# Performance work log

Measured on AMD Instinct MI355X. Metric: run time of the kernel, lower is better.

Reference implementation:

```python
import jax, jax.numpy as jnp
import numpy as np

INPUT_DIM = 512
HIDDEN_DIM = 512

def setup_inputs() -> dict:
    key = jax.random.key(0)
    ks = jax.random.split(key, 7)
    B, S = 4, 4096
    s = 1.0 / np.sqrt(INPUT_DIM)
    return {
        "x": jax.random.normal(ks[0], (B, INPUT_DIM, S), dtype=jnp.float32),
        "Wq": jax.random.uniform(ks[1], (INPUT_DIM, HIDDEN_DIM), jnp.float32, -s, s),
        "bq": jax.random.uniform(ks[2], (HIDDEN_DIM,), jnp.float32, -s, s),
        "Wk": jax.random.uniform(ks[3], (INPUT_DIM, HIDDEN_DIM), jnp.float32, -s, s),
        "bk": jax.random.uniform(ks[4], (HIDDEN_DIM,), jnp.float32, -s, s),
        "Wv": jax.random.uniform(ks[5], (INPUT_DIM, HIDDEN_DIM), jnp.float32, -s, s),
        "bv": jax.random.uniform(ks[6], (HIDDEN_DIM,), jnp.float32, -s, s),
    }

def reference(x, Wq, bq, Wk, bk, Wv, bv):
    # x: [B, input_dim, S] -> [B, S, input_dim]
    xt = jnp.swapaxes(x, 1, 2)
    q = xt @ Wq + bq  # [B, S, H]
    k = xt @ Wk + bk
    v = xt @ Wv + bv
    scale = 1.0 / jnp.sqrt(jnp.float32(HIDDEN_DIM))
    scores = jnp.einsum('bsh,bth->bst', q, k) * scale  # [B, S, S]
    attn = jax.nn.softmax(scores, axis=-1)
    out = jnp.einsum('bst,bth->bsh', attn, v)  # [B, S, H]
    return jnp.swapaxes(out, 1, 2)  # [B, H, S]
```

## Files before the change

### kernel.cpp

```cpp
#include <hip/hip_runtime.h>
#include <stdint.h>
#include <stddef.h>

typedef __attribute__((ext_vector_type(8))) short bf16x8;
typedef __attribute__((ext_vector_type(4))) short bf16x4;
typedef __attribute__((ext_vector_type(4))) float f32x4;

#define MFMA16x16x32 __builtin_amdgcn_mfma_f32_16x16x32_bf16
#define L2E 1.4426950408889634f

#define GLD_LDS(gp, lp)                                                              \
  __builtin_amdgcn_global_load_lds((const __attribute__((address_space(1))) void*)(gp), \
                                   (__attribute__((address_space(3))) void*)(lp), 16, 0, 0)

__device__ __forceinline__ short f2bf(float f) {
  union { float f; uint32_t u; } c; c.f = f;
  uint32_t r = c.u + 0x7fffu + ((c.u >> 16) & 1u);
  return (short)(r >> 16);
}

__global__ __launch_bounds__(256) void k_transpose_x(const float* __restrict__ x,
                                                     short* __restrict__ xt) {
  __shared__ float tile[32][33];
  const int b = blockIdx.z;
  const int s0 = blockIdx.x * 32, k0 = blockIdx.y * 32;
  const int tx = threadIdx.x, ty = threadIdx.y;
  const float* xp = x + ((size_t)b * 512 + k0) * 4096 + s0;
#pragma unroll
  for (int i = 0; i < 32; i += 8) tile[ty + i][tx] = xp[(size_t)(ty + i) * 4096 + tx];
  __syncthreads();
  short* op = xt + ((size_t)b * 4096 + s0) * 512 + k0;
#pragma unroll
  for (int i = 0; i < 32; i += 8) op[(size_t)(ty + i) * 512 + tx] = f2bf(tile[tx][ty + i]);
}

__global__ __launch_bounds__(256) void k_transpose_w(const float* __restrict__ w,
                                                     short* __restrict__ wt, float scale) {
  __shared__ float tile[32][33];
  const int h0 = blockIdx.x * 32, k0 = blockIdx.y * 32;
  const int tx = threadIdx.x, ty = threadIdx.y;
#pragma unroll
  for (int i = 0; i < 32; i += 8) tile[ty + i][tx] = w[(size_t)(k0 + ty + i) * 512 + h0 + tx];
  __syncthreads();
#pragma unroll
  for (int i = 0; i < 32; i += 8)
    wt[(size_t)(h0 + ty + i) * 512 + k0 + tx] = f2bf(tile[tx][ty + i] * scale);
}

__global__ __launch_bounds__(256) void k_proj_gemm(const short* __restrict__ A,
                                                   const short* __restrict__ Bt,
                                                   const float* __restrict__ bias,
                                                   short* __restrict__ outp,
                                                   float bscale, int vmode) {
  __shared__ short As[128 * 64];
  __shared__ short Bs[128 * 64];
  const int tid = threadIdx.x, lane = tid & 63, wave = tid >> 6;
  const int m0 = blockIdx.x * 128, h0 = blockIdx.y * 128;
  const int wm = wave >> 1, wn = wave & 1;

  f32x4 acc[4][4];
#pragma unroll
  for (int fh = 0; fh < 4; ++fh) {
    float bv = bias[h0 + 64 * wn + 16 * fh + (lane & 15)] * bscale;
#pragma unroll
    for (int fm = 0; fm < 4; ++fm) acc[fm][fh] = (f32x4){bv, bv, bv, bv};
  }

  for (int k0 = 0; k0 < 512; k0 += 64) {
#pragma unroll
    for (int it = 0; it < 4; ++it) {
      int p = it * 256 + tid;
      int row = p >> 3;
      int c = p & 7;
      int pc = c ^ (row & 7);
      bf16x8 va = *(const bf16x8*)(A + (size_t)(m0 + row) * 512 + k0 + c * 8);
      bf16x8 vb = *(const bf16x8*)(Bt + (size_t)(h0 + row) * 512 + k0 + c * 8);
      *(bf16x8*)(As + row * 64 + pc * 8) = va;
      *(bf16x8*)(Bs + row * 64 + pc * 8) = vb;
    }
    __syncthreads();
#pragma unroll
    for (int kk = 0; kk < 2; ++kk) {
      bf16x8 af[4], bfr[4];
#pragma unroll
      for (int f = 0; f < 4; ++f) {
        int ra = 64 * wm + 16 * f + (lane & 15);
        int ca = (4 * kk + (lane >> 4)) ^ (ra & 7);
        af[f] = *(const bf16x8*)(As + ra * 64 + ca * 8);
        int rb = 64 * wn + 16 * f + (lane & 15);
        int cb = (4 * kk + (lane >> 4)) ^ (rb & 7);
        bfr[f] = *(const bf16x8*)(Bs + rb * 64 + cb * 8);
      }
#pragma unroll
      for (int fm = 0; fm < 4; ++fm)
#pragma unroll
        for (int fh = 0; fh < 4; ++fh)
          acc[fm][fh] = MFMA16x16x32(af[fm], bfr[fh], acc[fm][fh], 0, 0, 0);
    }
    __syncthreads();
  }

  if (vmode == 0) {
#pragma unroll
    for (int fm = 0; fm < 4; ++fm) {
      int rbase = m0 + 64 * wm + 16 * fm + (lane >> 4) * 4;
#pragma unroll
      for (int fh = 0; fh < 4; ++fh) {
        int h = h0 + 64 * wn + 16 * fh + (lane & 15);
#pragma unroll
        for (int j = 0; j < 4; ++j)
          outp[(size_t)(rbase + j) * 512 + h] = f2bf(acc[fm][fh][j]);
      }
    }
  } else {
#pragma unroll
    for (int fm = 0; fm < 4; ++fm) {
      int m = m0 + 64 * wm + 16 * fm + (lane >> 4) * 4;
      int b = m >> 12, s = m & 4095;
#pragma unroll
      for (int fh = 0; fh < 4; ++fh) {
        int h = h0 + 64 * wn + 16 * fh + (lane & 15);
        bf16x4 v;
#pragma unroll
        for (int j = 0; j < 4; ++j) v[j] = f2bf(acc[fm][fh][j]);
        *(bf16x4*)(outp + ((size_t)b * 512 + h) * 4096 + s) = v;
      }
    }
  }
}

__global__ __launch_bounds__(512) void k_attn(const short* __restrict__ Qg,
                                              const short* __restrict__ Kg,
                                              const short* __restrict__ VTg,
                                              float* __restrict__ out) {
  __shared__ short Ks[64 * 512];
  __shared__ short Vs[512 * 64];
  __shared__ short Pbuf[64 * 64];
  __shared__ float Lfin[64];

  const int tid = threadIdx.x, lane = tid & 63, wave = tid >> 6;
  const int hi = lane >> 4, lo = lane & 15;
  const int b = blockIdx.y, qb = blockIdx.x;
  const int s0 = qb * 64;
  const int wm = wave >> 2, st = wave & 3;

  const short* Qb = Qg + (size_t)b * 4096 * 512;
  const short* Kb = Kg + (size_t)b * 4096 * 512;
  const short* VTb = VTg + (size_t)b * 512 * 4096;

  const short* kSrc[8];
  const short* vSrc[8];
#pragma unroll
  for (int it = 0; it < 8; ++it) {
    int r = it * 8 + wave;
    kSrc[it] = Kb + (size_t)r * 512 + (lane ^ wave) * 8;
    int h = it * 64 + wave * 8 + (lane >> 3);
    int c = (lane & 7) ^ (lane >> 3);
    vSrc[it] = VTb + (size_t)h * 4096 + c * 8;
  }

  bf16x8 qreg[2][16];
#pragma unroll
  for (int fa = 0; fa < 2; ++fa) {
    const short* qp = Qb + (size_t)(s0 + 32 * wm + 16 * fa + lo) * 512 + 8 * hi;
#pragma unroll
    for (int c = 0; c < 16; ++c) qreg[fa][c] = *(const bf16x8*)(qp + 32 * c);
  }

  bf16x8 onesB;
#pragma unroll
  for (int j = 0; j < 8; ++j) onesB[j] = (short)0x3F80;

  f32x4 of[2][8];
#pragma unroll
  for (int i = 0; i < 2; ++i)
#pragma unroll
    for (int j = 0; j < 8; ++j) of[i][j] = (f32x4){0.f, 0.f, 0.f, 0.f};
  f32x4 ol[2];
  ol[0] = (f32x4){0.f, 0.f, 0.f, 0.f};
  ol[1] = (f32x4){0.f, 0.f, 0.f, 0.f};

#pragma unroll
  for (int it = 0; it < 8; ++it) GLD_LDS(kSrc[it], &Ks[(it * 8 + wave) * 512]);
#pragma unroll
  for (int it = 0; it < 8; ++it) GLD_LDS(vSrc[it], &Vs[it * 4096 + wave * 512]);
  asm volatile("s_waitcnt vmcnt(0)" ::: "memory");
  asm volatile("s_waitcnt lgkmcnt(0)" ::: "memory");
  __builtin_amdgcn_s_barrier();
  asm volatile("" ::: "memory");

  for (int t = 0; t < 64; ++t) {
    f32x4 sf[2];
    sf[0] = (f32x4){0.f, 0.f, 0.f, 0.f};
    sf[1] = (f32x4){0.f, 0.f, 0.f, 0.f};
    __builtin_amdgcn_s_setprio(1);
#pragma unroll
    for (int kk = 0; kk < 16; ++kk) {
      int r = 16 * st + lo;
      bf16x8 kb = *(const bf16x8*)(Ks + r * 512 + ((4 * kk + hi) ^ (r & 7)) * 8);
      sf[0] = MFMA16x16x32(qreg[0][kk], kb, sf[0], 0, 0, 0);
      sf[1] = MFMA16x16x32(qreg[1][kk], kb, sf[1], 0, 0, 0);
    }
    __builtin_amdgcn_s_setprio(0);

#pragma unroll
    for (int fa = 0; fa < 2; ++fa) {
      int chunk = 2 * st + (lo >> 3);
#pragma unroll
      for (int j = 0; j < 4; ++j) {
        int q = 32 * wm + 16 * fa + 4 * hi + j;
        float p = exp2f(sf[fa][j] * L2E);
        Pbuf[q * 64 + (chunk ^ (q & 7)) * 8 + (lo & 7)] = f2bf(p);
      }
    }
    asm volatile("s_waitcnt vmcnt(0)" ::: "memory");
    asm volatile("s_waitcnt lgkmcnt(0)" ::: "memory");
    __builtin_amdgcn_s_barrier();
    asm volatile("" ::: "memory");

    if (t < 63) {
#pragma unroll
      for (int it = 0; it < 8; ++it) {
        kSrc[it] += 64 * 512;
        GLD_LDS(kSrc[it], &Ks[(it * 8 + wave) * 512]);
      }
    }

    __builtin_amdgcn_s_setprio(1);
#pragma unroll
    for (int ks = 0; ks < 2; ++ks) {
      bf16x8 pa[2];
#pragma unroll
      for (int fm = 0; fm < 2; ++fm) {
        int r = 32 * wm + 16 * fm + lo;
        pa[fm] = *(const bf16x8*)(Pbuf + r * 64 + ((4 * ks + hi) ^ (r & 7)) * 8);
      }
#pragma unroll
      for (int fh = 0; fh < 8; ++fh) {
        int n = 128 * st + 16 * fh + lo;
        bf16x8 vb = *(const bf16x8*)(Vs + n * 64 + ((4 * ks + hi) ^ (n & 7)) * 8);
#pragma unroll
        for (int fm = 0; fm < 2; ++fm) of[fm][fh] = MFMA16x16x32(pa[fm], vb, of[fm][fh], 0, 0, 0);
      }
      if (st == 0) {
        ol[0] = MFMA16x16x32(pa[0], onesB, ol[0], 0, 0, 0);
        ol[1] = MFMA16x16x32(pa[1], onesB, ol[1], 0, 0, 0);
      }
    }
    __builtin_amdgcn_s_setprio(0);
    asm volatile("s_waitcnt vmcnt(0)" ::: "memory");
    asm volatile("s_waitcnt lgkmcnt(0)" ::: "memory");
    __builtin_amdgcn_s_barrier();
    asm volatile("" ::: "memory");

    if (t < 63) {
#pragma unroll
      for (int it = 0; it < 8; ++it) {
        vSrc[it] += 64;
        GLD_LDS(vSrc[it], &Vs[it * 4096 + wave * 512]);
      }
    }
  }

  if (st == 0 && lo == 0) {
#pragma unroll
    for (int fm = 0; fm < 2; ++fm)
#pragma unroll
      for (int j = 0; j < 4; ++j) Lfin[32 * wm + 16 * fm + 4 * hi + j] = ol[fm][j];
  }
  __syncthreads();

#pragma unroll
  for (int fm = 0; fm < 2; ++fm) {
    int rb2 = 32 * wm + 16 * fm + hi * 4;
    float inv[4];
#pragma unroll
    for (int j = 0; j < 4; ++j) inv[j] = 1.f / Lfin[rb2 + j];
#pragma unroll
    for (int fh = 0; fh < 8; ++fh) {
      int h = 128 * st + 16 * fh + lo;
      f32x4 v;
#pragma unroll
      for (int j = 0; j < 4; ++j) v[j] = of[fm][fh][j] * inv[j];
      *(f32x4*)(out + ((size_t)b * 512 + h) * 4096 + s0 + rb2) = v;
    }
  }
}

extern "C" void kernel_launch(void* const* d_in, const int* in_sizes, int n_in,
                              void* d_out, int out_size, void* d_ws, size_t ws_size,
                              hipStream_t stream) {
  (void)in_sizes; (void)n_in; (void)out_size; (void)ws_size;
  const float* x = (const float*)d_in[0];
  const float* Wq = (const float*)d_in[1];
  const float* bq = (const float*)d_in[2];
  const float* Wk = (const float*)d_in[3];
  const float* bk = (const float*)d_in[4];
  const float* Wv = (const float*)d_in[5];
  const float* bv = (const float*)d_in[6];
  float* out = (float*)d_out;
  char* ws = (char*)d_ws;

  short* xt  = (short*)(ws + 0);
  short* qg  = (short*)(ws + 16777216);
  short* kg  = (short*)(ws + 33554432);
  short* vtg = (short*)(ws + 50331648);
  short* wqt = (short*)(ws + 67108864);
  short* wkt = (short*)(ws + 67633152);
  short* wvt = (short*)(ws + 68157440);

  const float scale = 0.04419417382415922f;

  k_transpose_x<<<dim3(128, 16, 4), dim3(32, 8), 0, stream>>>(x, xt);
  k_transpose_w<<<dim3(16, 16), dim3(32, 8), 0, stream>>>(Wq, wqt, scale);
  k_transpose_w<<<dim3(16, 16), dim3(32, 8), 0, stream>>>(Wk, wkt, 1.0f);
  k_transpose_w<<<dim3(16, 16), dim3(32, 8), 0, stream>>>(Wv, wvt, 1.0f);

  k_proj_gemm<<<dim3(128, 4), 256, 0, stream>>>(xt, wqt, bq, qg, scale, 0);
  k_proj_gemm<<<dim3(128, 4), 256, 0, stream>>>(xt, wkt, bk, kg, 1.0f, 0);
  k_proj_gemm<<<dim3(128, 4), 256, 0, stream>>>(xt, wvt, bv, vtg, 1.0f, 1);

  k_attn<<<dim3(64, 4), 512, 0, stream>>>(qg, kg, vtg, out);
}
```

Before: 255.3 us.

## Load V fragments directly from global into registers instead of via LDS

Drops the shared-memory staging buffer for V. Each wave now reads its V^T fragments straight from global memory into registers inside the PV loop, and the per-iteration V prefetch into LDS is gone. K source pointers are recomputed from a single base instead of being kept in eight registers, and sched_barrier calls are added before the workgroup barriers. This halves LDS usage and removes LDS traffic for V, but global loads now sit on the critical path right before the MFMAs with no prefetch. It also relies on L2 to serve the four query-block reuses of V.

After: 452.6 us. 1.77x slower.

```diff
diff --git a/kernel.cpp b/kernel.cpp
--- a/kernel.cpp
+++ b/kernel.cpp
@@ -134,7 +134,6 @@
                                               const short* __restrict__ VTg,
                                               float* __restrict__ out) {
   __shared__ short Ks[64 * 512];
-  __shared__ short Vs[512 * 64];
   __shared__ short Pbuf[64 * 64];
   __shared__ float Lfin[64];
 
@@ -148,16 +147,8 @@
   const short* Kb = Kg + (size_t)b * 4096 * 512;
   const short* VTb = VTg + (size_t)b * 512 * 4096;
 
-  const short* kSrc[8];
-  const short* vSrc[8];
-#pragma unroll
-  for (int it = 0; it < 8; ++it) {
-    int r = it * 8 + wave;
-    kSrc[it] = Kb + (size_t)r * 512 + (lane ^ wave) * 8;
-    int h = it * 64 + wave * 8 + (lane >> 3);
-    int c = (lane & 7) ^ (lane >> 3);
-    vSrc[it] = VTb + (size_t)h * 4096 + c * 8;
-  }
+  const short* kSrcBase = Kb + (size_t)wave * 512 + (lane ^ wave) * 8;
+  const short* vBase = VTb + (size_t)(128 * st + lo) * 4096 + 8 * hi;
 
   bf16x8 qreg[2][16];
 #pragma unroll
@@ -181,11 +172,11 @@
   ol[1] = (f32x4){0.f, 0.f, 0.f, 0.f};
 
 #pragma unroll
-  for (int it = 0; it < 8; ++it) GLD_LDS(kSrc[it], &Ks[(it * 8 + wave) * 512]);
-#pragma unroll
-  for (int it = 0; it < 8; ++it) GLD_LDS(vSrc[it], &Vs[it * 4096 + wave * 512]);
+  for (int it = 0; it < 8; ++it)
+    GLD_LDS(kSrcBase + (size_t)it * 8 * 512, &Ks[(it * 8 + wave) * 512]);
   asm volatile("s_waitcnt vmcnt(0)" ::: "memory");
   asm volatile("s_waitcnt lgkmcnt(0)" ::: "memory");
+  __builtin_amdgcn_sched_barrier(0);
   __builtin_amdgcn_s_barrier();
   asm volatile("" ::: "memory");
 
@@ -215,20 +206,24 @@
     }
     asm volatile("s_waitcnt vmcnt(0)" ::: "memory");
     asm volatile("s_waitcnt lgkmcnt(0)" ::: "memory");
+    __builtin_amdgcn_sched_barrier(0);
     __builtin_amdgcn_s_barrier();
     asm volatile("" ::: "memory");
 
     if (t < 63) {
-#pragma unroll
-      for (int it = 0; it < 8; ++it) {
-        kSrc[it] += 64 * 512;
-        GLD_LDS(kSrc[it], &Ks[(it * 8 + wave) * 512]);
-      }
+      const short* kSrc = kSrcBase + (size_t)(t + 1) * 64 * 512;
+#pragma unroll
+      for (int it = 0; it < 8; ++it)
+        GLD_LDS(kSrc + (size_t)it * 8 * 512, &Ks[(it * 8 + wave) * 512]);
     }
 
     __builtin_amdgcn_s_setprio(1);
 #pragma unroll
     for (int ks = 0; ks < 2; ++ks) {
+      bf16x8 vb[8];
+#pragma unroll
+      for (int fh = 0; fh < 8; ++fh)
+        vb[fh] = *(const bf16x8*)(vBase + (size_t)fh * 16 * 4096 + 64 * t + 32 * ks);
       bf16x8 pa[2];
 #pragma unroll
       for (int fm = 0; fm < 2; ++fm) {
@@ -236,30 +231,22 @@
         pa[fm] = *(const bf16x8*)(Pbuf + r * 64 + ((4 * ks + hi) ^ (r & 7)) * 8);
       }
 #pragma unroll
-      for (int fh = 0; fh < 8; ++fh) {
-        int n = 128 * st + 16 * fh + lo;
-        bf16x8 vb = *(const bf16x8*)(Vs + n * 64 + ((4 * ks + hi) ^ (n & 7)) * 8);
-#pragma unroll
-        for (int fm = 0; fm < 2; ++fm) of[fm][fh] = MFMA16x16x32(pa[fm], vb, of[fm][fh], 0, 0, 0);
-      }
+      for (int fh = 0; fh < 8; ++fh)
+#pragma unroll
+        for (int fm = 0; fm < 2; ++fm)
+          of[fm][fh] = MFMA16x16x32(pa[fm], vb[fh], of[fm][fh], 0, 0, 0);
       if (st == 0) {
         ol[0] = MFMA16x16x32(pa[0], onesB, ol[0], 0, 0, 0);
         ol[1] = MFMA16x16x32(pa[1], onesB, ol[1], 0, 0, 0);
       }
     }
     __builtin_amdgcn_s_setprio(0);
+
     asm volatile("s_waitcnt vmcnt(0)" ::: "memory");
     asm volatile("s_waitcnt lgkmcnt(0)" ::: "memory");
+    __builtin_amdgcn_sched_barrier(0);
     __builtin_amdgcn_s_barrier();
     asm volatile("" ::: "memory");
-
-    if (t < 63) {
-#pragma unroll
-      for (int it = 0; it < 8; ++it) {
-        vSrc[it] += 64;
-        GLD_LDS(vSrc[it], &Vs[it * 4096 + wave * 512]);
-      }
-    }
   }
 
   if (st == 0 && lo == 0) {
```
